# Kernel tuning notes

Measured on AMD Instinct MI355X. Metric: run time of the kernel, lower is better.

## Reference

```python
import jax, jax.numpy as jnp
import numpy as np

EPS = 1e-08


def squash(x):
    # x: [..., D]; scale by ||x||^2/(1+||x||^2) and normalize by ||x||
    lengths2 = jnp.sum(x * x, axis=-1, keepdims=True)
    lengths = jnp.sqrt(lengths2)
    return x * (lengths2 / (1.0 + lengths2)) / (lengths + EPS)


def setup_inputs() -> dict:
    key = jax.random.key(0)
    k1, = jax.random.split(key, 1)
    B, G, S, O, D = 32, 8, 1152, 10, 16
    u_predict = jax.random.normal(k1, (B, G, S, O, D), dtype=jnp.float32)
    b_param = jnp.zeros((G, 1, S, O), dtype=jnp.float32)
    return {"u_predict": u_predict, "b_param": b_param, "n_iterations": 3}


def reference(u_predict, b_param, n_iterations):
    B, G, S, O, D = u_predict.shape
    # b: expand param (G,1,S,O) -> (G,B,S,O), permute -> (B,G,S,O)
    b = jnp.transpose(jnp.broadcast_to(b_param, (G, B, S, O)), (1, 0, 2, 3))
    v = None
    for r in range(n_iterations):
        c = jax.nn.softmax(b, axis=3)[..., None]          # [B,G,S,O,1]
        s = jnp.sum(c * u_predict, axis=2)                # [B,G,O,D]
        v = squash(s)                                     # [B,G,O,D]
        if r < n_iterations - 1:
            # agreement: dot(u_predict, v) over D
            b = b + jnp.sum(u_predict * v[:, :, None], axis=-1)  # [B,G,S,O]
    return jnp.sum(v, axis=1)                             # [B,O,D]
```

## Files before the change

kernel.cpp:

```cpp
#include <hip/hip_runtime.h>

#define NB 32
#define NG 8
#define NS 1152
#define NO 10
#define ND 16
#define EPSV 1e-8f

#define THREADS 512
#define NWAVES (THREADS / 64)
#define GRPS (THREADS / 4)
#define NSTEPS (NS / GRPS)

__global__ __launch_bounds__(THREADS)
void AgreementRouting_72988674228343_kernel(const float* __restrict__ u,
                                            const float* __restrict__ b_param,
                                            const int* __restrict__ n_iter_p,
                                            float* __restrict__ out) {
    __shared__ float  b_lds[NS * NO];
    __shared__ float4 sred[NWAVES][NO][4];
    __shared__ float4 v_lds[NO][4];

    const int tid  = threadIdx.x;
    const int blk  = blockIdx.x;
    const int g    = blk & (NG - 1);
    const int bb   = blk >> 3;
    const int wave = tid >> 6;
    const int lane = tid & 63;
    const int d4   = tid & 3;
    const int grp  = tid >> 2;

    const int n_iter = n_iter_p[0];

    const float* bp = b_param + (size_t)g * (NS * NO);
    for (int i = tid; i < NS * NO; i += THREADS) b_lds[i] = bp[i];

    const float4* ub = (const float4*)u + (size_t)blk * (NS * NO * ND / 4);

    float4 v[NO];
    __syncthreads();

    for (int r = 0; r < n_iter; ++r) {
        float4 sacc[NO];
#pragma unroll
        for (int o = 0; o < NO; ++o) sacc[o] = make_float4(0.f, 0.f, 0.f, 0.f);

        for (int step = 0; step < NSTEPS; ++step) {
            const int s = step * GRPS + grp;
            const float4* row = ub + (size_t)s * (NO * 4) + d4;
            float4 uu[NO];
#pragma unroll
            for (int o = 0; o < NO; ++o) uu[o] = row[o * 4];

            float bnew[NO];
            if (r > 0) {
                float p[NO];
#pragma unroll
                for (int o = 0; o < NO; ++o)
                    p[o] = uu[o].x * v[o].x + uu[o].y * v[o].y +
                           uu[o].z * v[o].z + uu[o].w * v[o].w;
#pragma unroll
                for (int o = 0; o < NO; ++o) {
                    p[o] += __shfl_xor(p[o], 1);
                    p[o] += __shfl_xor(p[o], 2);
                    bnew[o] = b_lds[s * NO + o] + p[o];
                }
#pragma unroll
                for (int o = 0; o < NO; ++o)
                    if ((o & 3) == d4) b_lds[s * NO + o] = bnew[o];
            } else {
#pragma unroll
                for (int o = 0; o < NO; ++o) bnew[o] = b_lds[s * NO + o];
            }

            float m = bnew[0];
#pragma unroll
            for (int o = 1; o < NO; ++o) m = fmaxf(m, bnew[o]);
            float e[NO]; float ssum = 0.f;
#pragma unroll
            for (int o = 0; o < NO; ++o) { e[o] = __expf(bnew[o] - m); ssum += e[o]; }
            const float inv = 1.f / ssum;
#pragma unroll
            for (int o = 0; o < NO; ++o) {
                const float c = e[o] * inv;
                sacc[o].x += c * uu[o].x;
                sacc[o].y += c * uu[o].y;
                sacc[o].z += c * uu[o].z;
                sacc[o].w += c * uu[o].w;
            }
        }

#pragma unroll
        for (int o = 0; o < NO; ++o) {
#pragma unroll
            for (int mask = 4; mask <= 32; mask <<= 1) {
                sacc[o].x += __shfl_xor(sacc[o].x, mask);
                sacc[o].y += __shfl_xor(sacc[o].y, mask);
                sacc[o].z += __shfl_xor(sacc[o].z, mask);
                sacc[o].w += __shfl_xor(sacc[o].w, mask);
            }
        }
        if (lane < 4) {
#pragma unroll
            for (int o = 0; o < NO; ++o) sred[wave][o][lane] = sacc[o];
        }
        __syncthreads();

        if (tid < NO * 4) {
            const int o = tid >> 2, dd = tid & 3;
            float4 sv = sred[0][o][dd];
#pragma unroll
            for (int w = 1; w < NWAVES; ++w) {
                float4 t = sred[w][o][dd];
                sv.x += t.x; sv.y += t.y; sv.z += t.z; sv.w += t.w;
            }
            float q = sv.x * sv.x + sv.y * sv.y + sv.z * sv.z + sv.w * sv.w;
            q += __shfl_xor(q, 1);
            q += __shfl_xor(q, 2);
            const float len = sqrtf(q);
            const float f = (q / (1.f + q)) / (len + EPSV);
            const float4 vv = make_float4(sv.x * f, sv.y * f, sv.z * f, sv.w * f);
            v_lds[o][dd] = vv;
            if (r == n_iter - 1) {
                float* op = out + (size_t)bb * (NO * ND) + o * ND + dd * 4;
                atomicAdd(op + 0, vv.x);
                atomicAdd(op + 1, vv.y);
                atomicAdd(op + 2, vv.z);
                atomicAdd(op + 3, vv.w);
            }
        }
        __syncthreads();
#pragma unroll
        for (int o = 0; o < NO; ++o) v[o] = v_lds[o][d4];
    }
}

extern "C" void kernel_launch(void* const* d_in, const int* in_sizes, int n_in,
                              void* d_out, int out_size, void* d_ws, size_t ws_size,
                              hipStream_t stream) {
    const float* u   = (const float*)d_in[0];
    const float* bp  = (const float*)d_in[1];
    const int*   nit = (const int*)d_in[2];
    float* out = (float*)d_out;

    hipMemsetAsync(out, 0, (size_t)out_size * sizeof(float), stream);

    AgreementRouting_72988674228343_kernel<<<dim3(NB * NG), dim3(THREADS), 0, stream>>>(
        u, bp, nit, out);
}
```

Measured before the change: 318.7 us.

## Split routing into per-slice pass kernels and squash kernels across iterations

Replaces the single persistent block per (batch, group) with a grid over S-slices that computes partial weighted sums, followed by a small squash kernel per iteration. The routing logits are recomputed from b_param plus the dot product with a running sum of v, instead of being kept in LDS. This exposes much more parallelism to fill the GPU, at the cost of extra kernel launches and workspace traffic. The host loop is fixed at three iterations, so larger iteration counts would not be handled.

```diff
diff --git a/kernel.cpp b/kernel.cpp
--- a/kernel.cpp
+++ b/kernel.cpp
@@ -7,132 +7,114 @@
 #define ND 16
 #define EPSV 1e-8f
 
-#define THREADS 512
-#define NWAVES (THREADS / 64)
-#define GRPS (THREADS / 4)
-#define NSTEPS (NS / GRPS)
+#define RPB 64
+#define SP (NS / RPB)
+#define PTHREADS 256
 
-__global__ __launch_bounds__(THREADS)
-void AgreementRouting_72988674228343_kernel(const float* __restrict__ u,
-                                            const float* __restrict__ b_param,
-                                            const int* __restrict__ n_iter_p,
-                                            float* __restrict__ out) {
-    __shared__ float  b_lds[NS * NO];
-    __shared__ float4 sred[NWAVES][NO][4];
-    __shared__ float4 v_lds[NO][4];
-
+__global__ __launch_bounds__(PTHREADS)
+void ar_pass(const float* __restrict__ u, const float* __restrict__ b_param,
+             const float* __restrict__ vcum, float* __restrict__ ps,
+             const int* __restrict__ n_iter_p, int r)
+{
+    if (r >= n_iter_p[0]) return;
     const int tid  = threadIdx.x;
-    const int blk  = blockIdx.x;
-    const int g    = blk & (NG - 1);
-    const int bb   = blk >> 3;
+    const int sl   = blockIdx.x;
+    const int bg   = blockIdx.y;
+    const int g    = bg & (NG - 1);
+    const int d4   = tid & 3;
+    const int row  = tid >> 2;
+    const int s    = sl * RPB + row;
     const int wave = tid >> 6;
     const int lane = tid & 63;
-    const int d4   = tid & 3;
-    const int grp  = tid >> 2;
 
-    const int n_iter = n_iter_p[0];
+    const float4* urow = (const float4*)u + ((size_t)bg * NS + s) * (NO * 4) + d4;
+    const float4* vc   = (const float4*)vcum + (size_t)bg * (NO * 4) + d4;
+    const float*  bp   = b_param + (size_t)g * (NS * NO) + (size_t)s * NO;
 
-    const float* bp = b_param + (size_t)g * (NS * NO);
-    for (int i = tid; i < NS * NO; i += THREADS) b_lds[i] = bp[i];
+    float4 uu[NO];
+#pragma unroll
+    for (int o = 0; o < NO; ++o) uu[o] = urow[o * 4];
 
-    const float4* ub = (const float4*)u + (size_t)blk * (NS * NO * ND / 4);
+    float bnew[NO];
+#pragma unroll
+    for (int o = 0; o < NO; ++o) {
+        const float4 v4 = vc[o * 4];
+        float p = uu[o].x * v4.x + uu[o].y * v4.y + uu[o].z * v4.z + uu[o].w * v4.w;
+        p += __shfl_xor(p, 1);
+        p += __shfl_xor(p, 2);
+        bnew[o] = bp[o] + p;
+    }
 
-    float4 v[NO];
+    float m = bnew[0];
+#pragma unroll
+    for (int o = 1; o < NO; ++o) m = fmaxf(m, bnew[o]);
+    float ssum = 0.f;
+#pragma unroll
+    for (int o = 0; o < NO; ++o) { bnew[o] = __expf(bnew[o] - m); ssum += bnew[o]; }
+    const float inv = 1.f / ssum;
+
+#pragma unroll
+    for (int o = 0; o < NO; ++o) {
+        const float c = bnew[o] * inv;
+        uu[o].x *= c; uu[o].y *= c; uu[o].z *= c; uu[o].w *= c;
+    }
+
+#pragma unroll
+    for (int o = 0; o < NO; ++o) {
+#pragma unroll
+        for (int mask = 4; mask <= 32; mask <<= 1) {
+            uu[o].x += __shfl_xor(uu[o].x, mask);
+            uu[o].y += __shfl_xor(uu[o].y, mask);
+            uu[o].z += __shfl_xor(uu[o].z, mask);
+            uu[o].w += __shfl_xor(uu[o].w, mask);
+        }
+    }
+
+    __shared__ float4 red[PTHREADS / 64][NO][4];
+    if (lane < 4) {
+#pragma unroll
+        for (int o = 0; o < NO; ++o) red[wave][o][lane] = uu[o];
+    }
     __syncthreads();
 
-    for (int r = 0; r < n_iter; ++r) {
-        float4 sacc[NO];
+    if (tid < NO * 4) {
+        const int o = tid >> 2, dd = tid & 3;
+        float4 a = red[0][o][dd];
 #pragma unroll
-        for (int o = 0; o < NO; ++o) sacc[o] = make_float4(0.f, 0.f, 0.f, 0.f);
+        for (int w = 1; w < PTHREADS / 64; ++w) {
+            const float4 t = red[w][o][dd];
+            a.x += t.x; a.y += t.y; a.z += t.z; a.w += t.w;
+        }
+        ((float4*)ps)[(((size_t)bg * SP + sl) * NO + o) * 4 + dd] = a;
+    }
+}
 
-        for (int step = 0; step < NSTEPS; ++step) {
-            const int s = step * GRPS + grp;
-            const float4* row = ub + (size_t)s * (NO * 4) + d4;
-            float4 uu[NO];
+__global__ __launch_bounds__(192)
+void ar_squash(const float* __restrict__ ps, float* __restrict__ vcum,
+               float* __restrict__ out, const int* __restrict__ n_iter_p, int r)
+{
+    const int n = n_iter_p[0];
+    if (r >= n) return;
+    const int tid = threadIdx.x;
+    if (tid >= NO * ND) return;
+    const int bg = blockIdx.x;
+    const int o = tid >> 4, d = tid & 15;
+
+    const float* p = ps + ((size_t)bg * SP * NO + o) * ND + d;
+    float s = 0.f;
 #pragma unroll
-            for (int o = 0; o < NO; ++o) uu[o] = row[o * 4];
+    for (int sl = 0; sl < SP; ++sl) s += p[(size_t)sl * (NO * ND)];
 
-            float bnew[NO];
-            if (r > 0) {
-                float p[NO];
-#pragma unroll
-                for (int o = 0; o < NO; ++o)
-                    p[o] = uu[o].x * v[o].x + uu[o].y * v[o].y +
-                           uu[o].z * v[o].z + uu[o].w * v[o].w;
-#pragma unroll
-                for (int o = 0; o < NO; ++o) {
-                    p[o] += __shfl_xor(p[o], 1);
-                    p[o] += __shfl_xor(p[o], 2);
-                    bnew[o] = b_lds[s * NO + o] + p[o];
-                }
-#pragma unroll
-                for (int o = 0; o < NO; ++o)
-                    if ((o & 3) == d4) b_lds[s * NO + o] = bnew[o];
-            } else {
-#pragma unroll
-                for (int o = 0; o < NO; ++o) bnew[o] = b_lds[s * NO + o];
-            }
+    float q = s * s;
+    q += __shfl_xor(q, 1); q += __shfl_xor(q, 2);
+    q += __shfl_xor(q, 4); q += __shfl_xor(q, 8);
+    const float len = sqrtf(q);
+    const float f = (q / (1.f + q)) / (len + EPSV);
+    const float v = s * f;
 
-            float m = bnew[0];
-#pragma unroll
-            for (int o = 1; o < NO; ++o) m = fmaxf(m, bnew[o]);
-            float e[NO]; float ssum = 0.f;
-#pragma unroll
-            for (int o = 0; o < NO; ++o) { e[o] = __expf(bnew[o] - m); ssum += e[o]; }
-            const float inv = 1.f / ssum;
-#pragma unroll
-            for (int o = 0; o < NO; ++o) {
-                const float c = e[o] * inv;
-                sacc[o].x += c * uu[o].x;
-                sacc[o].y += c * uu[o].y;
-                sacc[o].z += c * uu[o].z;
-                sacc[o].w += c * uu[o].w;
-            }
-        }
-
-#pragma unroll
-        for (int o = 0; o < NO; ++o) {
-#pragma unroll
-            for (int mask = 4; mask <= 32; mask <<= 1) {
-                sacc[o].x += __shfl_xor(sacc[o].x, mask);
-                sacc[o].y += __shfl_xor(sacc[o].y, mask);
-                sacc[o].z += __shfl_xor(sacc[o].z, mask);
-                sacc[o].w += __shfl_xor(sacc[o].w, mask);
-            }
-        }
-        if (lane < 4) {
-#pragma unroll
-            for (int o = 0; o < NO; ++o) sred[wave][o][lane] = sacc[o];
-        }
-        __syncthreads();
-
-        if (tid < NO * 4) {
-            const int o = tid >> 2, dd = tid & 3;
-            float4 sv = sred[0][o][dd];
-#pragma unroll
-            for (int w = 1; w < NWAVES; ++w) {
-                float4 t = sred[w][o][dd];
-                sv.x += t.x; sv.y += t.y; sv.z += t.z; sv.w += t.w;
-            }
-            float q = sv.x * sv.x + sv.y * sv.y + sv.z * sv.z + sv.w * sv.w;
-            q += __shfl_xor(q, 1);
-            q += __shfl_xor(q, 2);
-            const float len = sqrtf(q);
-            const float f = (q / (1.f + q)) / (len + EPSV);
-            const float4 vv = make_float4(sv.x * f, sv.y * f, sv.z * f, sv.w * f);
-            v_lds[o][dd] = vv;
-            if (r == n_iter - 1) {
-                float* op = out + (size_t)bb * (NO * ND) + o * ND + dd * 4;
-                atomicAdd(op + 0, vv.x);
-                atomicAdd(op + 1, vv.y);
-                atomicAdd(op + 2, vv.z);
-                atomicAdd(op + 3, vv.w);
-            }
-        }
-        __syncthreads();
-#pragma unroll
-        for (int o = 0; o < NO; ++o) v[o] = v_lds[o][d4];
-    }
+    vcum[(size_t)bg * (NO * ND) + tid] += v;
+    if (r == n - 1)
+        atomicAdd(&out[(size_t)(bg >> 3) * (NO * ND) + tid], v);
 }
 
 extern "C" void kernel_launch(void* const* d_in, const int* in_sizes, int n_in,
@@ -141,10 +123,16 @@
     const float* u   = (const float*)d_in[0];
     const float* bp  = (const float*)d_in[1];
     const int*   nit = (const int*)d_in[2];
-    float* out = (float*)d_out;
+    float* out  = (float*)d_out;
+    float* ps   = (float*)d_ws;
+    float* vcum = ps + (size_t)NB * NG * SP * NO * ND;
 
     hipMemsetAsync(out, 0, (size_t)out_size * sizeof(float), stream);
+    hipMemsetAsync(vcum, 0, (size_t)NB * NG * NO * ND * sizeof(float), stream);
 
-    AgreementRouting_72988674228343_kernel<<<dim3(NB * NG), dim3(THREADS), 0, stream>>>(
-        u, bp, nit, out);
+    const dim3 pgrid(SP, NB * NG);
+    for (int r = 0; r < 3; ++r) {
+        ar_pass<<<pgrid, PTHREADS, 0, stream>>>(u, bp, vcum, ps, nit, r);
+        ar_squash<<<NB * NG, 192, 0, stream>>>(ps, vcum, out, nit, r);
+    }
 }
```

New measurement: 356.9 us. 1.12x slower.

## Split each routing task across a 16-block team with global-atomic iteration sync

Applied to the files above, without the earlier changes.

Each (batch, group) task is now split across 16 blocks, each handling 72 rows, so the work spreads over 512 persistent blocks instead of 256 blocks that each stream all 1152 rows serially. Partial s sums are combined with global atomics, and a closer block squashes them and publishes a cumulative v through a spin-waited flag for the next iteration. The logits b are recomputed from b_param plus the dot product with the accumulated v, so the per-row b state no longer needs to be kept in LDS. In exchange it adds inter-block spin synchronisation that relies on the whole grid being co-resident, a workspace memset, and atomics; the iteration count is capped at 8.

```diff
diff --git a/kernel.cpp b/kernel.cpp
--- a/kernel.cpp
+++ b/kernel.cpp
@@ -7,131 +7,171 @@
 #define ND 16
 #define EPSV 1e-8f
 
-#define THREADS 512
-#define NWAVES (THREADS / 64)
-#define GRPS (THREADS / 4)
-#define NSTEPS (NS / GRPS)
+#define THREADS 256
+#define TEAM 16
+#define SUBT 4
+#define GRID (TEAM * SUBT * 8)
+#define ROWS_PB (NS / TEAM)
+#define MAXIT 8
 
-__global__ __launch_bounds__(THREADS)
+__global__ __launch_bounds__(THREADS, 2)
 void AgreementRouting_72988674228343_kernel(const float* __restrict__ u,
-                                            const float* __restrict__ b_param,
+                                            const float* __restrict__ bparam,
                                             const int* __restrict__ n_iter_p,
-                                            float* __restrict__ out) {
-    __shared__ float  b_lds[NS * NO];
-    __shared__ float4 sred[NWAVES][NO][4];
-    __shared__ float4 v_lds[NO][4];
-
+                                            float* __restrict__ out,
+                                            float* __restrict__ s_glob,
+                                            float* __restrict__ vcum,
+                                            unsigned* __restrict__ cnt,
+                                            unsigned* __restrict__ flag)
+{
     const int tid  = threadIdx.x;
-    const int blk  = blockIdx.x;
-    const int g    = blk & (NG - 1);
-    const int bb   = blk >> 3;
+    const int x    = blockIdx.x & 7;
+    const int j    = blockIdx.x >> 3;
+    const int st   = j >> 4;
+    const int m    = j & 15;
+    const int d4   = tid & 3;
+    const int grp  = tid >> 2;
     const int wave = tid >> 6;
     const int lane = tid & 63;
-    const int d4   = tid & 3;
-    const int grp  = tid >> 2;
 
-    const int n_iter = n_iter_p[0];
+    int n = n_iter_p[0];
+    if (n > MAXIT) n = MAXIT;
 
-    const float* bp = b_param + (size_t)g * (NS * NO);
-    for (int i = tid; i < NS * NO; i += THREADS) b_lds[i] = bp[i];
+    __shared__ float4 sred[THREADS / 64][NO][4];
+    __shared__ int closer_lds;
 
-    const float4* ub = (const float4*)u + (size_t)blk * (NS * NO * ND / 4);
+    for (int round = 0; round < NB / SUBT; ++round) {
+        const int t  = round * SUBT + st;
+        const int bg = x + 8 * t;
+        const float* ub = u + (size_t)bg * (NS * NO * ND);
+        const float* bp = bparam + (size_t)x * (NS * NO);
+        float* sg_task = s_glob + (size_t)bg * (MAXIT * NO * ND);
+        float* vc_task = vcum + (size_t)bg * (NO * ND);
 
-    float4 v[NO];
-    __syncthreads();
-
-    for (int r = 0; r < n_iter; ++r) {
-        float4 sacc[NO];
-#pragma unroll
-        for (int o = 0; o < NO; ++o) sacc[o] = make_float4(0.f, 0.f, 0.f, 0.f);
-
-        for (int step = 0; step < NSTEPS; ++step) {
-            const int s = step * GRPS + grp;
-            const float4* row = ub + (size_t)s * (NO * 4) + d4;
-            float4 uu[NO];
-#pragma unroll
-            for (int o = 0; o < NO; ++o) uu[o] = row[o * 4];
-
-            float bnew[NO];
+        for (int r = 0; r < n; ++r) {
             if (r > 0) {
-                float p[NO];
-#pragma unroll
-                for (int o = 0; o < NO; ++o)
-                    p[o] = uu[o].x * v[o].x + uu[o].y * v[o].y +
-                           uu[o].z * v[o].z + uu[o].w * v[o].w;
-#pragma unroll
-                for (int o = 0; o < NO; ++o) {
-                    p[o] += __shfl_xor(p[o], 1);
-                    p[o] += __shfl_xor(p[o], 2);
-                    bnew[o] = b_lds[s * NO + o] + p[o];
+                if (tid == 0) {
+                    int spins = 0;
+                    while (__hip_atomic_load(&flag[bg], __ATOMIC_ACQUIRE,
+                                             __HIP_MEMORY_SCOPE_AGENT) < (unsigned)r) {
+                        __builtin_amdgcn_s_sleep(2);
+                        if (++spins > (1 << 27)) break;
+                    }
                 }
-#pragma unroll
-                for (int o = 0; o < NO; ++o)
-                    if ((o & 3) == d4) b_lds[s * NO + o] = bnew[o];
-            } else {
-#pragma unroll
-                for (int o = 0; o < NO; ++o) bnew[o] = b_lds[s * NO + o];
+                __syncthreads();
             }
 
-            float m = bnew[0];
+            float4 vc[NO];
+            const float4* vcp = (const float4*)vc_task + d4;
 #pragma unroll
-            for (int o = 1; o < NO; ++o) m = fmaxf(m, bnew[o]);
-            float e[NO]; float ssum = 0.f;
+            for (int o = 0; o < NO; ++o) vc[o] = vcp[o * 4];
+
+            float4 sacc[NO];
 #pragma unroll
-            for (int o = 0; o < NO; ++o) { e[o] = __expf(bnew[o] - m); ssum += e[o]; }
-            const float inv = 1.f / ssum;
+            for (int o = 0; o < NO; ++o) sacc[o] = make_float4(0.f, 0.f, 0.f, 0.f);
+
+            const int base = m * ROWS_PB;
+#pragma unroll
+            for (int rr = 0; rr < 2; ++rr) {
+                const int row = base + rr * 64 + grp;
+                const bool active = (rr == 0) || (grp < ROWS_PB - 64);
+                if (active) {
+                    const float4* up = (const float4*)(ub + (size_t)row * (NO * ND)) + d4;
+                    float4 uu[NO];
+#pragma unroll
+                    for (int o = 0; o < NO; ++o) uu[o] = up[o * 4];
+
+                    float bnew[NO];
+#pragma unroll
+                    for (int o = 0; o < NO; ++o) {
+                        float p = uu[o].x * vc[o].x + uu[o].y * vc[o].y +
+                                  uu[o].z * vc[o].z + uu[o].w * vc[o].w;
+                        p += __shfl_xor(p, 1);
+                        p += __shfl_xor(p, 2);
+                        bnew[o] = bp[row * NO + o] + p;
+                    }
+                    float mx = bnew[0];
+#pragma unroll
+                    for (int o = 1; o < NO; ++o) mx = fmaxf(mx, bnew[o]);
+                    float ss = 0.f;
+#pragma unroll
+                    for (int o = 0; o < NO; ++o) { bnew[o] = __expf(bnew[o] - mx); ss += bnew[o]; }
+                    const float inv = 1.f / ss;
+#pragma unroll
+                    for (int o = 0; o < NO; ++o) {
+                        const float c = bnew[o] * inv;
+                        sacc[o].x += c * uu[o].x;
+                        sacc[o].y += c * uu[o].y;
+                        sacc[o].z += c * uu[o].z;
+                        sacc[o].w += c * uu[o].w;
+                    }
+                }
+            }
+
 #pragma unroll
             for (int o = 0; o < NO; ++o) {
-                const float c = e[o] * inv;
-                sacc[o].x += c * uu[o].x;
-                sacc[o].y += c * uu[o].y;
-                sacc[o].z += c * uu[o].z;
-                sacc[o].w += c * uu[o].w;
+#pragma unroll
+                for (int mask = 4; mask <= 32; mask <<= 1) {
+                    sacc[o].x += __shfl_xor(sacc[o].x, mask);
+                    sacc[o].y += __shfl_xor(sacc[o].y, mask);
+                    sacc[o].z += __shfl_xor(sacc[o].z, mask);
+                    sacc[o].w += __shfl_xor(sacc[o].w, mask);
+                }
+            }
+            if (lane < 4) {
+#pragma unroll
+                for (int o = 0; o < NO; ++o) sred[wave][o][lane] = sacc[o];
+            }
+            __syncthreads();
+
+            if (tid < NO * 4) {
+                const int o = tid >> 2, dd = tid & 3;
+                float4 a = sred[0][o][dd];
+#pragma unroll
+                for (int w = 1; w < THREADS / 64; ++w) {
+                    const float4 q = sred[w][o][dd];
+                    a.x += q.x; a.y += q.y; a.z += q.z; a.w += q.w;
+                }
+                float* dst = sg_task + r * (NO * ND) + o * ND + dd * 4;
+                atomicAdd(dst + 0, a.x);
+                atomicAdd(dst + 1, a.y);
+                atomicAdd(dst + 2, a.z);
+                atomicAdd(dst + 3, a.w);
+            }
+            __syncthreads();
+
+            if (tid == 0) {
+                __threadfence();
+                const unsigned old = __hip_atomic_fetch_add(&cnt[bg * MAXIT + r], 1u,
+                                                            __ATOMIC_ACQ_REL,
+                                                            __HIP_MEMORY_SCOPE_AGENT);
+                closer_lds = (old == TEAM - 1);
+            }
+            __syncthreads();
+
+            if (closer_lds) {
+                if (tid < NO * ND) {
+                    const float s = __hip_atomic_load(&sg_task[r * (NO * ND) + tid],
+                                                      __ATOMIC_RELAXED,
+                                                      __HIP_MEMORY_SCOPE_AGENT);
+                    float q = s * s;
+                    q += __shfl_xor(q, 1); q += __shfl_xor(q, 2);
+                    q += __shfl_xor(q, 4); q += __shfl_xor(q, 8);
+                    const float len = sqrtf(q);
+                    const float f = (q / (1.f + q)) / (len + EPSV);
+                    const float v = s * f;
+                    vc_task[tid] += v;
+                    if (r == n - 1)
+                        atomicAdd(&out[(size_t)t * (NO * ND) + tid], v);
+                }
+                __syncthreads();
+                if (tid == 0) {
+                    __threadfence();
+                    __hip_atomic_store(&flag[bg], (unsigned)(r + 1),
+                                       __ATOMIC_RELEASE, __HIP_MEMORY_SCOPE_AGENT);
+                }
             }
         }
-
-#pragma unroll
-        for (int o = 0; o < NO; ++o) {
-#pragma unroll
-            for (int mask = 4; mask <= 32; mask <<= 1) {
-                sacc[o].x += __shfl_xor(sacc[o].x, mask);
-                sacc[o].y += __shfl_xor(sacc[o].y, mask);
-                sacc[o].z += __shfl_xor(sacc[o].z, mask);
-                sacc[o].w += __shfl_xor(sacc[o].w, mask);
-            }
-        }
-        if (lane < 4) {
-#pragma unroll
-            for (int o = 0; o < NO; ++o) sred[wave][o][lane] = sacc[o];
-        }
-        __syncthreads();
-
-        if (tid < NO * 4) {
-            const int o = tid >> 2, dd = tid & 3;
-            float4 sv = sred[0][o][dd];
-#pragma unroll
-            for (int w = 1; w < NWAVES; ++w) {
-                float4 t = sred[w][o][dd];
-                sv.x += t.x; sv.y += t.y; sv.z += t.z; sv.w += t.w;
-            }
-            float q = sv.x * sv.x + sv.y * sv.y + sv.z * sv.z + sv.w * sv.w;
-            q += __shfl_xor(q, 1);
-            q += __shfl_xor(q, 2);
-            const float len = sqrtf(q);
-            const float f = (q / (1.f + q)) / (len + EPSV);
-            const float4 vv = make_float4(sv.x * f, sv.y * f, sv.z * f, sv.w * f);
-            v_lds[o][dd] = vv;
-            if (r == n_iter - 1) {
-                float* op = out + (size_t)bb * (NO * ND) + o * ND + dd * 4;
-                atomicAdd(op + 0, vv.x);
-                atomicAdd(op + 1, vv.y);
-                atomicAdd(op + 2, vv.z);
-                atomicAdd(op + 3, vv.w);
-            }
-        }
-        __syncthreads();
-#pragma unroll
-        for (int o = 0; o < NO; ++o) v[o] = v_lds[o][d4];
     }
 }
 
@@ -143,8 +183,16 @@
     const int*   nit = (const int*)d_in[2];
     float* out = (float*)d_out;
 
+    const int NTASK = NB * NG;
+    float*    s_glob = (float*)d_ws;
+    float*    vcum   = s_glob + (size_t)NTASK * MAXIT * NO * ND;
+    unsigned* cnt    = (unsigned*)(vcum + (size_t)NTASK * NO * ND);
+    unsigned* flag   = cnt + (size_t)NTASK * MAXIT;
+    const size_t ws_bytes = (size_t)((char*)(flag + NTASK) - (char*)d_ws);
+
+    hipMemsetAsync(d_ws, 0, ws_bytes, stream);
     hipMemsetAsync(out, 0, (size_t)out_size * sizeof(float), stream);
 
-    AgreementRouting_72988674228343_kernel<<<dim3(NB * NG), dim3(THREADS), 0, stream>>>(
-        u, bp, nit, out);
+    AgreementRouting_72988674228343_kernel<<<dim3(GRID), dim3(THREADS), 0, stream>>>(
+        u, bp, nit, out, s_glob, vcum, cnt, flag);
 }
```

Result: slower. 1.228 ms (+285.4%).

## Double-buffer u tiles in LDS via async global_load_lds with cumulative v

Applied to the files above, without the earlier changes.

Streams u through a double-buffered, XOR-swizzled LDS tile using global_load_lds, so the next tile's load overlaps compute on the current one. The routing logits are no longer written back. Each pass instead rebuilds them from the original b plus a dot product with the running sum of all previous v, which drops the LDS writes of b. Threads are remapped to 8 lanes per row with float2 elements, and launch bounds now request 2 blocks per SM. The cost is a block-wide barrier on every tile and about 80KB of LDS per block, which may limit occupancy.

```diff
diff --git a/kernel.cpp b/kernel.cpp
--- a/kernel.cpp
+++ b/kernel.cpp
@@ -1,4 +1,5 @@
 #include <hip/hip_runtime.h>
+#include <stdint.h>
 
 #define NB 32
 #define NG 8
@@ -8,130 +9,150 @@
 #define EPSV 1e-8f
 
 #define THREADS 512
-#define NWAVES (THREADS / 64)
-#define GRPS (THREADS / 4)
-#define NSTEPS (NS / GRPS)
+#define RT 64
+#define ROWB (NO * ND * 4)
+#define TILEB (RT * ROWB)
+#define NH (NS / RT)
 
-__global__ __launch_bounds__(THREADS)
+typedef const __attribute__((address_space(1))) uint32_t* gp1_t;
+typedef __attribute__((address_space(3))) uint32_t* lp3_t;
+
+__global__ __launch_bounds__(THREADS, 2)
 void AgreementRouting_72988674228343_kernel(const float* __restrict__ u,
-                                            const float* __restrict__ b_param,
+                                            const float* __restrict__ bparam,
                                             const int* __restrict__ n_iter_p,
-                                            float* __restrict__ out) {
+                                            float* __restrict__ out)
+{
+    __shared__ char   lds_u[2][TILEB];
     __shared__ float  b_lds[NS * NO];
-    __shared__ float4 sred[NWAVES][NO][4];
-    __shared__ float4 v_lds[NO][4];
+    __shared__ float2 vcum_lds[NO * 8];
+    __shared__ float2 sred[8][NO * 8];
 
     const int tid  = threadIdx.x;
-    const int blk  = blockIdx.x;
-    const int g    = blk & (NG - 1);
-    const int bb   = blk >> 3;
+    const int bg   = blockIdx.x;
+    const int g    = bg & 7;
+    const int bb   = bg >> 3;
+    const int l8   = tid & 7;
+    const int rl   = tid >> 3;
     const int wave = tid >> 6;
     const int lane = tid & 63;
-    const int d4   = tid & 3;
-    const int grp  = tid >> 2;
 
-    const int n_iter = n_iter_p[0];
+    const int n = n_iter_p[0];
 
-    const float* bp = b_param + (size_t)g * (NS * NO);
+    const char*  ug = (const char*)u + (size_t)bg * ((size_t)NS * ROWB);
+    const float* bp = bparam + (size_t)g * (NS * NO);
+
     for (int i = tid; i < NS * NO; i += THREADS) b_lds[i] = bp[i];
+    if (tid < NO * 8) vcum_lds[tid] = make_float2(0.f, 0.f);
 
-    const float4* ub = (const float4*)u + (size_t)blk * (NS * NO * ND / 4);
+    auto stage = [&](int h, int c) {
+#pragma unroll
+        for (int k = 0; k < 5; ++k) {
+            const int S   = tid * 16 + k * 8192;
+            const int r   = S / ROWB;
+            const int src = S ^ ((r & 7) << 4);
+            __builtin_amdgcn_global_load_lds(
+                (gp1_t)(ug + (size_t)h * TILEB + src),
+                (lp3_t)(&lds_u[c][S]), 16, 0, 0);
+        }
+    };
 
-    float4 v[NO];
+    stage(0, 0);
     __syncthreads();
 
-    for (int r = 0; r < n_iter; ++r) {
-        float4 sacc[NO];
+    int pb = 0;
+    const int swz = (rl & 7) << 4;
+
+    for (int r = 0; r < n; ++r) {
+        float2 vc[NO];
 #pragma unroll
-        for (int o = 0; o < NO; ++o) sacc[o] = make_float4(0.f, 0.f, 0.f, 0.f);
+        for (int o = 0; o < NO; ++o) vc[o] = vcum_lds[o * 8 + l8];
 
-        for (int step = 0; step < NSTEPS; ++step) {
-            const int s = step * GRPS + grp;
-            const float4* row = ub + (size_t)s * (NO * 4) + d4;
-            float4 uu[NO];
+        float2 sacc[NO];
 #pragma unroll
-            for (int o = 0; o < NO; ++o) uu[o] = row[o * 4];
+        for (int o = 0; o < NO; ++o) sacc[o] = make_float2(0.f, 0.f);
+
+        for (int h = 0; h < NH; ++h) {
+            const int cur = pb, nxt = pb ^ 1;
+            if ((h + 1 < NH) | (r + 1 < n))
+                stage((h + 1 < NH) ? h + 1 : 0, nxt);
+
+            const char* base = lds_u[cur] + rl * ROWB;
+            float2 uu[NO];
+#pragma unroll
+            for (int o = 0; o < NO; ++o)
+                uu[o] = *(const float2*)(base + ((o * 64 + l8 * 8) ^ swz));
 
             float bnew[NO];
+            const float* brow = &b_lds[(h * RT + rl) * NO];
             if (r > 0) {
-                float p[NO];
-#pragma unroll
-                for (int o = 0; o < NO; ++o)
-                    p[o] = uu[o].x * v[o].x + uu[o].y * v[o].y +
-                           uu[o].z * v[o].z + uu[o].w * v[o].w;
 #pragma unroll
                 for (int o = 0; o < NO; ++o) {
-                    p[o] += __shfl_xor(p[o], 1);
-                    p[o] += __shfl_xor(p[o], 2);
-                    bnew[o] = b_lds[s * NO + o] + p[o];
+                    float p = uu[o].x * vc[o].x + uu[o].y * vc[o].y;
+                    p += __shfl_xor(p, 1);
+                    p += __shfl_xor(p, 2);
+                    p += __shfl_xor(p, 4);
+                    bnew[o] = brow[o] + p;
                 }
-#pragma unroll
-                for (int o = 0; o < NO; ++o)
-                    if ((o & 3) == d4) b_lds[s * NO + o] = bnew[o];
             } else {
 #pragma unroll
-                for (int o = 0; o < NO; ++o) bnew[o] = b_lds[s * NO + o];
+                for (int o = 0; o < NO; ++o) bnew[o] = brow[o];
             }
 
-            float m = bnew[0];
+            float mx = bnew[0];
 #pragma unroll
-            for (int o = 1; o < NO; ++o) m = fmaxf(m, bnew[o]);
-            float e[NO]; float ssum = 0.f;
+            for (int o = 1; o < NO; ++o) mx = fmaxf(mx, bnew[o]);
+            float ss = 0.f;
 #pragma unroll
-            for (int o = 0; o < NO; ++o) { e[o] = __expf(bnew[o] - m); ssum += e[o]; }
-            const float inv = 1.f / ssum;
+            for (int o = 0; o < NO; ++o) { bnew[o] = __expf(bnew[o] - mx); ss += bnew[o]; }
+            const float inv = 1.f / ss;
 #pragma unroll
             for (int o = 0; o < NO; ++o) {
-                const float c = e[o] * inv;
+                const float c = bnew[o] * inv;
                 sacc[o].x += c * uu[o].x;
                 sacc[o].y += c * uu[o].y;
-                sacc[o].z += c * uu[o].z;
-                sacc[o].w += c * uu[o].w;
             }
+            pb ^= 1;
+            __syncthreads();
         }
 
 #pragma unroll
         for (int o = 0; o < NO; ++o) {
 #pragma unroll
-            for (int mask = 4; mask <= 32; mask <<= 1) {
+            for (int mask = 8; mask <= 32; mask <<= 1) {
                 sacc[o].x += __shfl_xor(sacc[o].x, mask);
                 sacc[o].y += __shfl_xor(sacc[o].y, mask);
-                sacc[o].z += __shfl_xor(sacc[o].z, mask);
-                sacc[o].w += __shfl_xor(sacc[o].w, mask);
             }
         }
-        if (lane < 4) {
+        if (lane < 8) {
 #pragma unroll
-            for (int o = 0; o < NO; ++o) sred[wave][o][lane] = sacc[o];
+            for (int o = 0; o < NO; ++o) sred[wave][o * 8 + lane] = sacc[o];
         }
         __syncthreads();
 
-        if (tid < NO * 4) {
-            const int o = tid >> 2, dd = tid & 3;
-            float4 sv = sred[0][o][dd];
+        if (tid < NO * 8) {
+            float2 s2 = sred[0][tid];
 #pragma unroll
-            for (int w = 1; w < NWAVES; ++w) {
-                float4 t = sred[w][o][dd];
-                sv.x += t.x; sv.y += t.y; sv.z += t.z; sv.w += t.w;
+            for (int w = 1; w < 8; ++w) {
+                const float2 t = sred[w][tid];
+                s2.x += t.x; s2.y += t.y;
             }
-            float q = sv.x * sv.x + sv.y * sv.y + sv.z * sv.z + sv.w * sv.w;
+            float q = s2.x * s2.x + s2.y * s2.y;
             q += __shfl_xor(q, 1);
             q += __shfl_xor(q, 2);
+            q += __shfl_xor(q, 4);
             const float len = sqrtf(q);
             const float f = (q / (1.f + q)) / (len + EPSV);
-            const float4 vv = make_float4(sv.x * f, sv.y * f, sv.z * f, sv.w * f);
-            v_lds[o][dd] = vv;
-            if (r == n_iter - 1) {
-                float* op = out + (size_t)bb * (NO * ND) + o * ND + dd * 4;
+            const float2 vv = make_float2(s2.x * f, s2.y * f);
+            const float2 c2 = vcum_lds[tid];
+            vcum_lds[tid] = make_float2(c2.x + vv.x, c2.y + vv.y);
+            if (r == n - 1) {
+                float* op = out + (size_t)bb * (NO * ND) + tid * 2;
                 atomicAdd(op + 0, vv.x);
                 atomicAdd(op + 1, vv.y);
-                atomicAdd(op + 2, vv.z);
-                atomicAdd(op + 3, vv.w);
             }
         }
         __syncthreads();
-#pragma unroll
-        for (int o = 0; o < NO; ++o) v[o] = v_lds[o][d4];
     }
 }
 
```

Result: slower. 336.7 us (+5.6%).
